# Kernel tuning notes

Measured on AMD Instinct MI355X. Metric: run time of the kernel, lower is better.

Reference implementation:

```python
import jax, jax.numpy as jnp
import numpy as np

EPS = 1e-5

def _layernorm(x):
    # elementwise_affine=False LayerNorm over last dim
    mu = jnp.mean(x, axis=-1, keepdims=True)
    var = jnp.mean(jnp.square(x - mu), axis=-1, keepdims=True)
    return (x - mu) / jnp.sqrt(var + EPS)

def setup_inputs() -> dict:
    key = jax.random.key(0)
    B, I, H = 16384, 512, 512
    ks = jax.random.split(key, 10)
    std = 1.0 / np.sqrt(H)
    u = lambda k, shape: jax.random.uniform(k, shape, jnp.float32, -std, std)
    return {
        "x": jax.random.normal(ks[0], (B, I), jnp.float32),
        "h": jax.random.normal(ks[1], (B, H), jnp.float32),
        "W_i2h": u(ks[2], (2 * H, I)),
        "b_i2h": u(ks[3], (2 * H,)),
        "W_h2h": u(ks[4], (2 * H, H)),
        "b_h2h": u(ks[5], (2 * H,)),
        "W_hatW": u(ks[6], (H, I)),
        "b_hatW": u(ks[7], (H,)),
        "W_hatU": u(ks[8], (H, H)),
        "b_hatU": u(ks[9], (H,)),
    }

def reference(x, h, W_i2h, b_i2h, W_h2h, b_h2h, W_hatW, b_hatW, W_hatU, b_hatU):
    H = W_hatU.shape[0]
    i2h = _layernorm(x @ W_i2h.T + b_i2h)   # [B, 2H]
    h2h = _layernorm(h @ W_h2h.T + b_h2h)   # [B, 2H]
    gates = jax.nn.sigmoid(i2h + h2h)
    z_t = gates[:, :H]
    r_t = gates[:, -H:]
    h_hat_a = _layernorm(x @ W_hatW.T + b_hatW)
    h_hat_b = _layernorm(h @ W_hatU.T + b_hatU)
    h_hat = jnp.tanh(h_hat_a + r_t * h_hat_b)
    h_t = (1.0 - z_t) * h + z_t * h_hat
    return h_t
```

## Files before the change

kernel.cpp:

```cpp
#include <hip/hip_runtime.h>
#include <hip/hip_bf16.h>


using f32x4 = __attribute__((ext_vector_type(4))) float;
using s16x8 = __attribute__((ext_vector_type(8))) short;
typedef __attribute__((ext_vector_type(8))) unsigned short u16x8;

#define WB_OFF   0ull
#define GB_OFF   1572864ull

__device__ __forceinline__ void async_load16(const void* g, void* l) {
  __builtin_amdgcn_global_load_lds(
      (const __attribute__((address_space(1))) unsigned int*)g,
      (__attribute__((address_space(3))) unsigned int*)l, 16, 0, 0);
}

__device__ __forceinline__ float bfraw2f(unsigned short u) {
  union { unsigned int i; float f; } c;
  c.i = ((unsigned int)u) << 16;
  return c.f;
}

__global__ __launch_bounds__(256) void convert_w_kernel(
    const float* __restrict__ w0, const float* __restrict__ w1,
    const float* __restrict__ w2, const float* __restrict__ w3,
    __hip_bfloat16* __restrict__ dst)
{
  const size_t i = (size_t)blockIdx.x * 256 + threadIdx.x;
  const float* src;
  __hip_bfloat16* d;
  size_t o;
  if (i < 131072ull)      { src = w0; d = dst;            o = i; }
  else if (i < 262144ull) { src = w1; d = dst + 524288;   o = i - 131072ull; }
  else if (i < 327680ull) { src = w2; d = dst + 1048576;  o = i - 262144ull; }
  else                    { src = w3; d = dst + 1310720;  o = i - 327680ull; }
  const float4 v = *(const float4*)(src + 4 * o);
  __hip_bfloat16 t4[4] = {__float2bfloat16(v.x), __float2bfloat16(v.y),
                          __float2bfloat16(v.z), __float2bfloat16(v.w)};
  *(uint2*)(d + 4 * o) = *(const uint2*)t4;
}

#define B_BASE 131072

__device__ __forceinline__ void stage_B(const char* base, char* slot,
                                        int koff, int wave, int lane) {
#pragma unroll
  for (int i = 0; i < 2; ++i) {
    const int c = wave * 2 + i;
    const int row  = c * 16 + (lane >> 2);
    const int colb = ((lane & 3) * 16) ^ (((lane >> 3) & 3) << 4);
    async_load16(base + (size_t)row * 1024 + koff + colb,
                 slot + c * 1024 + lane * 16);
  }
}

__device__ __forceinline__ void cvt_write8(void* dst, const float4& f0,
                                           const float4& f1) {
  union { s16x8 v; __hip_bfloat16 b[8]; } u;
  u.b[0] = __float2bfloat16(f0.x); u.b[1] = __float2bfloat16(f0.y);
  u.b[2] = __float2bfloat16(f0.z); u.b[3] = __float2bfloat16(f0.w);
  u.b[4] = __float2bfloat16(f1.x); u.b[5] = __float2bfloat16(f1.y);
  u.b[6] = __float2bfloat16(f1.z); u.b[7] = __float2bfloat16(f1.w);
  *(s16x8*)dst = u.v;
}

__global__ __launch_bounds__(512, 2) void gemm_kernel(
    const float* __restrict__ xf,
    const float* __restrict__ hf,
    const __hip_bfloat16* __restrict__ Wb,
    __hip_bfloat16* __restrict__ G)
{
  const int bid   = blockIdx.x;
  const int type  = bid & 1;
  const int mband = bid >> 1;
  const int m0    = mband * 128;
  const float* Af = (type ? hf : xf) + (size_t)m0 * 512;

  __shared__ __align__(16) char lds[163840];

  const int tid  = threadIdx.x;
  const int lane = tid & 63;
  const int wave = tid >> 6;
  const int wm = wave >> 2, wn = wave & 3;

  const int lk  = (lane >> 4) * 16;
  const int lr  = lane & 15;
  const int rdk = lk ^ (((lr >> 1) & 3) << 4);

  auto rdA = [&](int kt, int fm) {
    return *(const s16x8*)(lds + kt * 8192 +
                           (wm * 64 + fm * 16 + lr) * 64 + rdk);
  };
  auto rdB = [&](int slot, int fn) {
    return *(const s16x8*)(lds + B_BASE + slot * 16384 +
                           (wn * 64 + fn * 16 + lr) * 64 + rdk);
  };

  const int ntl0 = type ? 4 : 0;
  const char* Bb0 = (const char*)Wb + (size_t)ntl0 * 256 * 1024;

  stage_B(Bb0, lds + B_BASE, 0, wave, lane);

  const int arow = tid >> 2;
  const int alin = (tid & 3) * 16;
  const int acb  = alin ^ (((arow >> 1) & 3) << 4);
  const float* abase = Af + (size_t)arow * 512 + (alin >> 1);
  char* const awr = lds + arow * 64 + acb;

  float4 hA, hB;
  {
    const float4 a0 = *(const float4*)(abase);
    const float4 a1 = *(const float4*)(abase + 4);
    hA = *(const float4*)(abase + 32);
    hB = *(const float4*)(abase + 36);
    cvt_write8(awr, a0, a1);
  }

  {
    const int ntl1 = type ? 5 : 1;
    const char* BbN = (const char*)Wb + (size_t)ntl1 * 256 * 1024;

    f32x4 acc[4][4];
#pragma unroll
    for (int a = 0; a < 4; ++a)
#pragma unroll
      for (int b = 0; b < 4; ++b) acc[a][b] = (f32x4){0.f, 0.f, 0.f, 0.f};

#pragma unroll
    for (int kt = 0; kt < 16; ++kt) {
      asm volatile("s_waitcnt vmcnt(0) lgkmcnt(0)" ::: "memory");
      __builtin_amdgcn_s_barrier();

      if (kt <= 14) cvt_write8(awr + (kt + 1) * 8192, hA, hB);

      const int slot = kt & 1;
      s16x8 b[4], a[4];
#pragma unroll
      for (int fn = 0; fn < 4; ++fn) b[fn] = rdB(slot, fn);
#pragma unroll
      for (int fm = 0; fm < 4; ++fm) a[fm] = rdA(kt, fm);

      if (kt < 15)
        stage_B(Bb0, lds + B_BASE + ((kt + 1) & 1) * 16384, (kt + 1) * 64,
                wave, lane);
      else
        stage_B(BbN, lds + B_BASE, 0, wave, lane);

      if (kt <= 13) {
        hA = *(const float4*)(abase + (kt + 2) * 32);
        hB = *(const float4*)(abase + (kt + 2) * 32 + 4);
      }

      __builtin_amdgcn_s_setprio(1);
#pragma unroll
      for (int fm = 0; fm < 4; ++fm)
#pragma unroll
        for (int fn = 0; fn < 4; ++fn)
          acc[fm][fn] = __builtin_amdgcn_mfma_f32_16x16x32_bf16(
              a[fm], b[fn], acc[fm][fn], 0, 0, 0);
      __builtin_amdgcn_s_setprio(0);
    }

    const int n0 = ntl0 * 256;
    const int mbase = m0 + wm * 64 + ((lane >> 4) << 2);
    const int nbase = n0 + wn * 64 + lr;
#pragma unroll
    for (int fm = 0; fm < 4; ++fm)
#pragma unroll
      for (int fn = 0; fn < 4; ++fn)
#pragma unroll
        for (int r = 0; r < 4; ++r)
          G[(size_t)(mbase + fm * 16 + r) * 3072 + nbase + fn * 16] =
              __float2bfloat16(acc[fm][fn][r]);
  }

  for (int i = 1; i < 6; ++i) {
    const int ntl = (i < 4) ? (type ? i + 4 : i) : (type ? i + 6 : i + 4);
    const int ntlN = (i + 1 < 4) ? (type ? i + 5 : i + 1)
                                 : (type ? i + 7 : i + 5);
    const char* Bb  = (const char*)Wb + (size_t)ntl * 256 * 1024;
    const char* BbN = (const char*)Wb + (size_t)(i < 5 ? ntlN : ntl) * 256 * 1024;

    f32x4 acc[4][4];
#pragma unroll
    for (int a = 0; a < 4; ++a)
#pragma unroll
      for (int b = 0; b < 4; ++b) acc[a][b] = (f32x4){0.f, 0.f, 0.f, 0.f};

    s16x8 aC[4];
#pragma unroll
    for (int kt = 0; kt < 16; ++kt) {
      asm volatile("s_waitcnt vmcnt(0)" ::: "memory");
      __builtin_amdgcn_s_barrier();

      if (kt < 15)
        stage_B(Bb, lds + B_BASE + ((kt + 1) & 1) * 16384, (kt + 1) * 64,
                wave, lane);
      else if (i < 5)
        stage_B(BbN, lds + B_BASE, 0, wave, lane);

      const int slot = kt & 1;
      s16x8 b[4];
#pragma unroll
      for (int fn = 0; fn < 4; ++fn) b[fn] = rdB(slot, fn);
      if (kt == 0) {
#pragma unroll
        for (int fm = 0; fm < 4; ++fm) aC[fm] = rdA(0, fm);
      }

      __builtin_amdgcn_s_setprio(1);
#pragma unroll
      for (int fm = 0; fm < 2; ++fm)
#pragma unroll
        for (int fn = 0; fn < 4; ++fn)
          acc[fm][fn] = __builtin_amdgcn_mfma_f32_16x16x32_bf16(
              aC[fm], b[fn], acc[fm][fn], 0, 0, 0);

      s16x8 aN[4];
      if (kt < 15) {
#pragma unroll
        for (int fm = 0; fm < 4; ++fm) aN[fm] = rdA(kt + 1, fm);
      }

#pragma unroll
      for (int fm = 2; fm < 4; ++fm)
#pragma unroll
        for (int fn = 0; fn < 4; ++fn)
          acc[fm][fn] = __builtin_amdgcn_mfma_f32_16x16x32_bf16(
              aC[fm], b[fn], acc[fm][fn], 0, 0, 0);
      __builtin_amdgcn_s_setprio(0);

      if (kt < 15) {
#pragma unroll
        for (int fm = 0; fm < 4; ++fm) aC[fm] = aN[fm];
      }
    }

    const int n0 = ntl * 256;
    const int mbase = m0 + wm * 64 + ((lane >> 4) << 2);
    const int nbase = n0 + wn * 64 + lr;
#pragma unroll
    for (int fm = 0; fm < 4; ++fm)
#pragma unroll
      for (int fn = 0; fn < 4; ++fn)
#pragma unroll
        for (int r = 0; r < 4; ++r)
          G[(size_t)(mbase + fm * 16 + r) * 3072 + nbase + fn * 16] =
              __float2bfloat16(acc[fm][fn][r]);
  }
}

__global__ __launch_bounds__(256) void ln_gate_kernel(
    const __hip_bfloat16* __restrict__ G, const float* __restrict__ h,
    const float* __restrict__ b0, const float* __restrict__ b1,
    const float* __restrict__ b2, const float* __restrict__ b3,
    float* __restrict__ out)
{
  const int w = threadIdx.x >> 6;
  const int L = threadIdx.x & 63;
  const int row = blockIdx.x * 4 + w;
  const unsigned short* g = (const unsigned short*)(G + (size_t)row * 3072);

  __shared__ float zr[4][1024];
  float* const zw = zr[w];

  float v0[16], v1[16];
  {
    const u16x8 a0 = *(const u16x8*)(g + 16 * L);
    const u16x8 a1 = *(const u16x8*)(g + 16 * L + 8);
    const u16x8 c0 = *(const u16x8*)(g + 1024 + 16 * L);
    const u16x8 c1 = *(const u16x8*)(g + 1024 + 16 * L + 8);
#pragma unroll
    for (int q = 0; q < 4; ++q) {
      const float4 f0 = *(const float4*)(b0 + 16 * L + 4 * q);
      const float4 f1 = *(const float4*)(b1 + 16 * L + 4 * q);
      const float bb0[4] = {f0.x, f0.y, f0.z, f0.w};
      const float bb1[4] = {f1.x, f1.y, f1.z, f1.w};
#pragma unroll
      for (int j = 0; j < 4; ++j) {
        const int k = 4 * q + j;
        const unsigned short ua = (k < 8) ? a0[k] : a1[k - 8];
        const unsigned short uc = (k < 8) ? c0[k] : c1[k - 8];
        v0[k] = bfraw2f(ua) + bb0[j];
        v1[k] = bfraw2f(uc) + bb1[j];
      }
    }
  }
  float4 s = make_float4(0.f, 0.f, 0.f, 0.f);
#pragma unroll
  for (int k = 0; k < 16; ++k) {
    s.x += v0[k]; s.y += v0[k] * v0[k];
    s.z += v1[k]; s.w += v1[k] * v1[k];
  }
#pragma unroll
  for (int off = 1; off < 64; off <<= 1) {
    s.x += __shfl_xor(s.x, off);
    s.y += __shfl_xor(s.y, off);
    s.z += __shfl_xor(s.z, off);
    s.w += __shfl_xor(s.w, off);
  }
  const float mu0 = s.x * (1.f / 1024.f);
  const float mu1 = s.z * (1.f / 1024.f);
  const float rs0 = rsqrtf(s.y * (1.f / 1024.f) - mu0 * mu0 + 1e-5f);
  const float rs1 = rsqrtf(s.w * (1.f / 1024.f) - mu1 * mu1 + 1e-5f);

#pragma unroll
  for (int k = 0; k < 16; ++k) {
    const float pre = (v0[k] - mu0) * rs0 + (v1[k] - mu1) * rs1;
    zw[k * 64 + L] = 1.f / (1.f + __expf(-pre));
  }

  float v2[8], v3[8];
  {
    const u16x8 a = *(const u16x8*)(g + 2048 + 8 * L);
    const u16x8 c = *(const u16x8*)(g + 2560 + 8 * L);
#pragma unroll
    for (int q = 0; q < 2; ++q) {
      const float4 f2 = *(const float4*)(b2 + 8 * L + 4 * q);
      const float4 f3 = *(const float4*)(b3 + 8 * L + 4 * q);
      const float bb2[4] = {f2.x, f2.y, f2.z, f2.w};
      const float bb3[4] = {f3.x, f3.y, f3.z, f3.w};
#pragma unroll
      for (int j = 0; j < 4; ++j) {
        const int k = 4 * q + j;
        v2[k] = bfraw2f(a[k]) + bb2[j];
        v3[k] = bfraw2f(c[k]) + bb3[j];
      }
    }
  }
  float4 t = make_float4(0.f, 0.f, 0.f, 0.f);
#pragma unroll
  for (int k = 0; k < 8; ++k) {
    t.x += v2[k]; t.y += v2[k] * v2[k];
    t.z += v3[k]; t.w += v3[k] * v3[k];
  }
#pragma unroll
  for (int off = 1; off < 64; off <<= 1) {
    t.x += __shfl_xor(t.x, off);
    t.y += __shfl_xor(t.y, off);
    t.z += __shfl_xor(t.z, off);
    t.w += __shfl_xor(t.w, off);
  }
  const float mu2 = t.x * (1.f / 512.f);
  const float mu3 = t.z * (1.f / 512.f);
  const float rs2 = rsqrtf(t.y * (1.f / 512.f) - mu2 * mu2 + 1e-5f);
  const float rs3 = rsqrtf(t.w * (1.f / 512.f) - mu3 * mu3 + 1e-5f);

  asm volatile("s_waitcnt lgkmcnt(0)" ::: "memory");

  const float4 h0 = *(const float4*)(h + (size_t)row * 512 + 8 * L);
  const float4 h1 = *(const float4*)(h + (size_t)row * 512 + 8 * L + 4);
  const float hv[8] = {h0.x, h0.y, h0.z, h0.w, h1.x, h1.y, h1.z, h1.w};

  float o[8];
#pragma unroll
  for (int k = 0; k < 8; ++k) {
    const int c  = 8 * L + k;
    const float z  = zw[(c & 15) * 64 + (c >> 4)];
    const float rr = zw[((512 + c) & 15) * 64 + ((512 + c) >> 4)];
    const float ha  = (v2[k] - mu2) * rs2;
    const float hbv = (v3[k] - mu3) * rs3;
    const float hhat = tanhf(ha + rr * hbv);
    o[k] = (1.f - z) * hv[k] + z * hhat;
  }
  *(float4*)(out + (size_t)row * 512 + 8 * L)     = make_float4(o[0], o[1], o[2], o[3]);
  *(float4*)(out + (size_t)row * 512 + 8 * L + 4) = make_float4(o[4], o[5], o[6], o[7]);
}

extern "C" void kernel_launch(void* const* d_in, const int* in_sizes, int n_in,
                              void* d_out, int out_size, void* d_ws, size_t ws_size,
                              hipStream_t stream) {
  (void)in_sizes; (void)n_in; (void)out_size; (void)ws_size;
  const float* x      = (const float*)d_in[0];
  const float* h      = (const float*)d_in[1];
  const float* W_i2h  = (const float*)d_in[2];
  const float* b_i2h  = (const float*)d_in[3];
  const float* W_h2h  = (const float*)d_in[4];
  const float* b_h2h  = (const float*)d_in[5];
  const float* W_hatW = (const float*)d_in[6];
  const float* b_hatW = (const float*)d_in[7];
  const float* W_hatU = (const float*)d_in[8];
  const float* b_hatU = (const float*)d_in[9];
  float* out = (float*)d_out;
  __hip_bfloat16* ws = (__hip_bfloat16*)d_ws;

  convert_w_kernel<<<1536, 256, 0, stream>>>(W_i2h, W_h2h, W_hatW, W_hatU,
                                             ws + WB_OFF);
  gemm_kernel<<<256, 512, 0, stream>>>(x, h, ws + WB_OFF, ws + GB_OFF);
  ln_gate_kernel<<<4096, 256, 0, stream>>>(ws + GB_OFF, h, b_i2h, b_h2h,
                                           b_hatW, b_hatU, out);
}
```

Before: 105.7 us.

## Load B fragments directly from global into registers for later N-tiles

For the N-tile loop after the first, B operand fragments are now read straight from global memory into registers and software-pipelined one k-step ahead, instead of being staged through double-buffered LDS with async loads and per-step barriers. This removes the workgroup barriers and LDS traffic in the inner loop, since A is already resident in LDS. The cost is that each wave fetches its own B fragments with uncoalesced 16-byte accesses from global/L2, which increases cache traffic and exposes global latency with only one step of prefetch.

Measured after the change: 134.7 us. 1.27x slower.

```diff
diff --git a/kernel.cpp b/kernel.cpp
--- a/kernel.cpp
+++ b/kernel.cpp
@@ -40,6 +40,7 @@
   *(uint2*)(d + 4 * o) = *(const uint2*)t4;
 }
 
+
 #define B_BASE 131072
 
 __device__ __forceinline__ void stage_B(const char* base, char* slot,
@@ -117,9 +118,6 @@
   }
 
   {
-    const int ntl1 = type ? 5 : 1;
-    const char* BbN = (const char*)Wb + (size_t)ntl1 * 256 * 1024;
-
     f32x4 acc[4][4];
 #pragma unroll
     for (int a = 0; a < 4; ++a)
@@ -143,8 +141,6 @@
       if (kt < 15)
         stage_B(Bb0, lds + B_BASE + ((kt + 1) & 1) * 16384, (kt + 1) * 64,
                 wave, lane);
-      else
-        stage_B(BbN, lds + B_BASE, 0, wave, lane);
 
       if (kt <= 13) {
         hA = *(const float4*)(abase + (kt + 2) * 32);
@@ -174,12 +170,12 @@
               __float2bfloat16(acc[fm][fn][r]);
   }
 
+  const char* bglane = (const char*)Wb + (size_t)(wn * 64 + lr) * 1024 +
+                       (lane >> 4) * 16;
+
   for (int i = 1; i < 6; ++i) {
     const int ntl = (i < 4) ? (type ? i + 4 : i) : (type ? i + 6 : i + 4);
-    const int ntlN = (i + 1 < 4) ? (type ? i + 5 : i + 1)
-                                 : (type ? i + 7 : i + 5);
-    const char* Bb  = (const char*)Wb + (size_t)ntl * 256 * 1024;
-    const char* BbN = (const char*)Wb + (size_t)(i < 5 ? ntlN : ntl) * 256 * 1024;
+    const char* bgl = bglane + (size_t)ntl * 262144;
 
     f32x4 acc[4][4];
 #pragma unroll
@@ -187,26 +183,16 @@
 #pragma unroll
       for (int b = 0; b < 4; ++b) acc[a][b] = (f32x4){0.f, 0.f, 0.f, 0.f};
 
-    s16x8 aC[4];
+    s16x8 aC[4], bC[4];
+#pragma unroll
+    for (int fm = 0; fm < 4; ++fm) aC[fm] = rdA(0, fm);
+#pragma unroll
+    for (int fn = 0; fn < 4; ++fn)
+      bC[fn] = *(const s16x8*)(bgl + fn * 16384);
+
 #pragma unroll
     for (int kt = 0; kt < 16; ++kt) {
-      asm volatile("s_waitcnt vmcnt(0)" ::: "memory");
-      __builtin_amdgcn_s_barrier();
-
-      if (kt < 15)
-        stage_B(Bb, lds + B_BASE + ((kt + 1) & 1) * 16384, (kt + 1) * 64,
-                wave, lane);
-      else if (i < 5)
-        stage_B(BbN, lds + B_BASE, 0, wave, lane);
-
-      const int slot = kt & 1;
-      s16x8 b[4];
-#pragma unroll
-      for (int fn = 0; fn < 4; ++fn) b[fn] = rdB(slot, fn);
-      if (kt == 0) {
-#pragma unroll
-        for (int fm = 0; fm < 4; ++fm) aC[fm] = rdA(0, fm);
-      }
+      s16x8 aN[4], bN[4];
 
       __builtin_amdgcn_s_setprio(1);
 #pragma unroll
@@ -214,10 +200,12 @@
 #pragma unroll
         for (int fn = 0; fn < 4; ++fn)
           acc[fm][fn] = __builtin_amdgcn_mfma_f32_16x16x32_bf16(
-              aC[fm], b[fn], acc[fm][fn], 0, 0, 0);
-
-      s16x8 aN[4];
+              aC[fm], bC[fn], acc[fm][fn], 0, 0, 0);
+
       if (kt < 15) {
+#pragma unroll
+        for (int fn = 0; fn < 4; ++fn)
+          bN[fn] = *(const s16x8*)(bgl + fn * 16384 + (kt + 1) * 64);
 #pragma unroll
         for (int fm = 0; fm < 4; ++fm) aN[fm] = rdA(kt + 1, fm);
       }
@@ -227,12 +215,12 @@
 #pragma unroll
         for (int fn = 0; fn < 4; ++fn)
           acc[fm][fn] = __builtin_amdgcn_mfma_f32_16x16x32_bf16(
-              aC[fm], b[fn], acc[fm][fn], 0, 0, 0);
+              aC[fm], bC[fn], acc[fm][fn], 0, 0, 0);
       __builtin_amdgcn_s_setprio(0);
 
       if (kt < 15) {
 #pragma unroll
-        for (int fm = 0; fm < 4; ++fm) aC[fm] = aN[fm];
+        for (int q = 0; q < 4; ++q) { aC[q] = aN[q]; bC[q] = bN[q]; }
       }
     }
 
```
